# Performance work log

Measured on AMD Instinct MI355X. Metric: run time of the kernel, lower is better.

## Reference

```python
import jax, jax.numpy as jnp
import numpy as np

BATCH = 16384
IN = 1024
OUT = 1024
SIGMA_MIN = 0.1
SIGMA_MAX = 1.0


def setup_inputs() -> dict:
    key = jax.random.key(0)
    k0, k1, k2, k3 = jax.random.split(key, 4)
    x = jax.random.normal(k0, (BATCH, IN), dtype=jnp.float32)
    # torch init: triu(randn) -> upper-triangular reflector banks
    U = jnp.triu(jax.random.normal(k1, (IN, IN), dtype=jnp.float32))
    V = jnp.triu(jax.random.normal(k2, (OUT, OUT), dtype=jnp.float32))
    p = 0.001 * jax.random.normal(k3, (min(IN, OUT),), dtype=jnp.float32)
    bias = jnp.zeros((OUT,), dtype=jnp.float32)
    return {"x": x, "U": U, "V": V, "p": p, "bias": bias}


def _hprod_step(x, u):
    # u has zeros in its first i entries (triu row i), so the full-vector
    # form equals torch's sliced Hprod on the last k = n - i columns.
    alpha = 2.0 * (x @ u) / jnp.dot(u, u)          # [bs]
    return x - alpha[:, None] * u[None, :], None   # rank-1 update


def reference(x, U, V, p, bias):
    r = (SIGMA_MAX - SIGMA_MIN) / 2.0
    sigma_mean = SIGMA_MIN + r
    # mask enforces torch slice semantics (entries below diag never used)
    Um = U * jnp.triu(jnp.ones_like(U))
    Vm = V * jnp.triu(jnp.ones_like(V))
    # Umultiply: reflectors i = 0 .. n_U-1 in order (sequential recurrence)
    x, _ = jax.lax.scan(_hprod_step, x, Um)
    # Sigma: diagonal scaling (square case IN == OUT)
    sigmas = 2.0 * r * (jax.nn.sigmoid(p) - 0.5) + sigma_mean
    x = x * sigmas[None, :]
    # Vmultiply: reflectors i = n_V-1 .. 0 (reverse order)
    x, _ = jax.lax.scan(_hprod_step, x, Vm[::-1])
    return x + bias
```

## Files before the change

### kernel.cpp

```cpp
#include <hip/hip_runtime.h>
#include <stdint.h>

typedef __attribute__((ext_vector_type(8))) short short8;
typedef __attribute__((ext_vector_type(4))) float f32x4;

#define NN 1024
#define NBATCH 16384
#define ME ((size_t)NN * NN)
#define AS1 (const __attribute__((address_space(1))) void*)
#define AS3 (__attribute__((address_space(3))) void*)

__device__ __forceinline__ unsigned short f32_to_bf16_rne(float f) {
  unsigned int u = __float_as_uint(f);
  unsigned int r = (u + 0x7fffu + ((u >> 16) & 1u)) >> 16;
  return (unsigned short)r;
}

__device__ __forceinline__ unsigned int pack2bf(float lo, float hi) {
  return (unsigned int)f32_to_bf16_rne(lo) | ((unsigned int)f32_to_bf16_rne(hi) << 16);
}

__device__ __forceinline__ void split_bf16(float x, unsigned short& h, unsigned short& l) {
  h = f32_to_bf16_rne(x);
  float hf = __uint_as_float((unsigned int)h << 16);
  l = f32_to_bf16_rne(x - hf);
}

__device__ __forceinline__ float allsum64(float x) {
  x += __int_as_float(__builtin_amdgcn_update_dpp(0, __float_as_int(x), 0xB1, 0xF, 0xF, true));
  x += __int_as_float(__builtin_amdgcn_update_dpp(0, __float_as_int(x), 0x4E, 0xF, 0xF, true));
  x += __int_as_float(__builtin_amdgcn_update_dpp(0, __float_as_int(x), 0x141, 0xF, 0xF, true));
  x += __int_as_float(__builtin_amdgcn_update_dpp(0, __float_as_int(x), 0x140, 0xF, 0xF, true));
#if __has_builtin(__builtin_amdgcn_permlane16_swap) && __has_builtin(__builtin_amdgcn_permlane32_swap)
  {
    auto r16 = __builtin_amdgcn_permlane16_swap(__float_as_uint(x), __float_as_uint(x), false, false);
    x = __uint_as_float(r16[0]) + __uint_as_float(r16[1]);
    auto r32 = __builtin_amdgcn_permlane32_swap(__float_as_uint(x), __float_as_uint(x), false, false);
    x = __uint_as_float(r32[0]) + __uint_as_float(r32[1]);
  }
#else
  x += __int_as_float(__builtin_amdgcn_ds_swizzle(__float_as_int(x), 0x401F));
  x += __shfl_xor(x, 32);
#endif
  return x;
}

__global__ __launch_bounds__(256) void prep_kernel(
    const float* __restrict__ U, const float* __restrict__ V,
    const float* __restrict__ p, float* __restrict__ tau_u,
    float* __restrict__ tau_v, float* __restrict__ sigmas) {
  int wave = threadIdx.x >> 6, lane = threadIdx.x & 63;
  int row = blockIdx.x * 4 + wave;
  if (row < 2048) {
    const float* u = (row < NN) ? (U + (size_t)row * NN) : (V + (size_t)(row - NN) * NN);
    float s = 0.f;
#pragma unroll
    for (int t = 0; t < 16; ++t) { float a = u[lane + (t << 6)]; s += a * a; }
    s = allsum64(s);
    if (lane == 0) {
      float tau = 2.0f / s;
      if (row < NN) tau_u[row] = tau;
      else tau_v[row - NN] = tau;
    }
  } else if (row < 2064) {
    int j = ((row - 2048) << 6) + lane;
    float pj = p[j];
    float sg = 1.0f / (1.0f + expf(-pj));
    sigmas[j] = 0.9f * (sg - 0.5f) + 0.55f;
  }
}

__global__ __launch_bounds__(256) void castx_kernel(
    const float* __restrict__ X, unsigned short* __restrict__ Xb) {
  const size_t n4 = (size_t)NBATCH * NN / 4;
  for (size_t i = (size_t)blockIdx.x * 256 + threadIdx.x; i < n4; i += (size_t)gridDim.x * 256) {
    float4 v = reinterpret_cast<const float4*>(X)[i];
    uint2 o;
    o.x = pack2bf(v.x, v.y);
    o.y = pack2bf(v.z, v.w);
    reinterpret_cast<uint2*>(Xb)[i] = o;
  }
}

__global__ __launch_bounds__(64) void gram_t8_kernel(
    const float* __restrict__ U, const float* __restrict__ V,
    const float* __restrict__ tau_u, const float* __restrict__ tau_v,
    float* __restrict__ T8all) {
  __shared__ float G[64];
  const int blk = blockIdx.x;
  const int lane = threadIdx.x;
  const float* bank;
  int rbase, rsign, st;
  if (blk < 128) { bank = U; rbase = 8 * blk; rsign = 1; st = 8 * blk; }
  else { int s = blk - 128; bank = V; rbase = 1023 - 8 * s; rsign = -1; st = 1016 - 8 * s; }

  if (lane < 28) {
    int j = 1, k = 0, t = lane;
    for (int jj = 1; jj < 8; ++jj) {
      int lo = jj * (jj - 1) / 2, hi = jj * (jj + 1) / 2;
      if (t >= lo && t < hi) { j = jj; k = t - lo; }
    }
    const float* rk = bank + (size_t)(rbase + rsign * k) * NN;
    const float* rj = bank + (size_t)(rbase + rsign * j) * NN;
    float acc = 0.f;
    for (int i = st >> 2; i < 256; ++i) {
      float4 a = *reinterpret_cast<const float4*>(rk + 4 * i);
      float4 b = *reinterpret_cast<const float4*>(rj + 4 * i);
      acc += a.x * b.x + a.y * b.y + a.z * b.z + a.w * b.w;
    }
    G[k * 8 + j] = acc;
  }
  __syncthreads();

  if (lane < 8) {
    float Tr[8];
#pragma unroll
    for (int j = 0; j < 8; ++j) Tr[j] = 0.f;
#pragma unroll
    for (int j = 0; j < 8; ++j) {
      int grow = rbase + rsign * j;
      float tj = (blk < 128) ? tau_u[grow] : tau_v[grow];
      float a = 0.f;
#pragma unroll
      for (int k = 0; k < 8; ++k) {
        if (k < j) a += Tr[k] * G[k * 8 + j];
      }
      Tr[j] = (lane == j) ? tj : (-tj * a);
    }
#pragma unroll
    for (int j = 0; j < 8; ++j) T8all[(size_t)blk * 64 + lane * 8 + j] = Tr[j];
  }
}

__global__ __launch_bounds__(256) void splity_kernel(
    const float* __restrict__ U, const float* __restrict__ V,
    unsigned short* __restrict__ Yhi, unsigned short* __restrict__ Ylo,
    unsigned short* __restrict__ YThi, unsigned short* __restrict__ YTlo) {
  __shared__ float ys[128][129];
  const int tid = threadIdx.x;
  const int c = blockIdx.x >> 3, et = blockIdx.x & 7;
  const int half = tid & 1;
  const int slot = tid >> 1;
  const int e0 = et << 7;
  const int grow = (c < 8) ? ((c << 7) + slot) : (1023 - ((c - 8) << 7) - slot);
  const float* src = ((c < 8) ? U : V) + (size_t)grow * NN + e0 + (half << 6);
#pragma unroll
  for (int i = 0; i < 16; ++i) {
    float4 v4 = *reinterpret_cast<const float4*>(src + (i << 2));
    const int kk = (half << 6) + (i << 2);
    ys[slot][kk + 0] = v4.x; ys[slot][kk + 1] = v4.y;
    ys[slot][kk + 2] = v4.z; ys[slot][kk + 3] = v4.w;
  }
  __syncthreads();
  {
    const size_t rbase = ((size_t)(c * 128 + slot)) * NN + e0 + (half << 6);
#pragma unroll
    for (int i = 0; i < 16; ++i) {
      const int kk = (half << 6) + (i << 2);
      ushort4 h4, l4;
      split_bf16(ys[slot][kk + 0], h4.x, l4.x);
      split_bf16(ys[slot][kk + 1], h4.y, l4.y);
      split_bf16(ys[slot][kk + 2], h4.z, l4.z);
      split_bf16(ys[slot][kk + 3], h4.w, l4.w);
      *reinterpret_cast<ushort4*>(&Yhi[rbase + (i << 2)]) = h4;
      *reinterpret_cast<ushort4*>(&Ylo[rbase + (i << 2)]) = l4;
    }
  }
  {
    const int e = slot;
    const size_t tbase = ((size_t)c * 1024 + e0 + e) * 128 + (half << 6);
#pragma unroll
    for (int i = 0; i < 16; ++i) {
      const int k0 = (half << 6) + (i << 2);
      ushort4 h4, l4;
      split_bf16(ys[k0 + 0][e], h4.x, l4.x);
      split_bf16(ys[k0 + 1][e], h4.y, l4.y);
      split_bf16(ys[k0 + 2][e], h4.z, l4.z);
      split_bf16(ys[k0 + 3][e], h4.w, l4.w);
      *reinterpret_cast<ushort4*>(&YThi[tbase + (i << 2)]) = h4;
      *reinterpret_cast<ushort4*>(&YTlo[tbase + (i << 2)]) = l4;
    }
  }
}

#define LDK 40
#define BM 128
#define BN 128
#define BK 32

__global__ __launch_bounds__(256) void gramt_kernel(
    const unsigned short* __restrict__ Yhi, const unsigned short* __restrict__ Ylo,
    float* __restrict__ Gp) {
  const int tid = threadIdx.x;
  const int c = blockIdx.x >> 3, ks = blockIdx.x & 7;
  const bool productive = (c < 8) ? (ks >= c) : (ks >= 7 - (c - 8));
  if (!productive) {
    float4 z = {0.f, 0.f, 0.f, 0.f};
    float4* dst = reinterpret_cast<float4*>(Gp + (((size_t)c * 8 + ks) << 14));
    for (int i = tid; i < 4096; i += 256) dst[i] = z;
    return;
  }
  __shared__ unsigned short Hs[128 * LDK];
  __shared__ unsigned short Ls[128 * LDK];
  const int lane = tid & 63, wave = tid >> 6;
  const int wm = wave & 1, wn = wave >> 1;
  const int srow = tid >> 1, scol = (tid & 1) << 4;
  const unsigned short* ph = Yhi + ((size_t)(c * 128 + srow)) * NN + ks * 128 + scol;
  const unsigned short* pl = Ylo + ((size_t)(c * 128 + srow)) * NN + ks * 128 + scol;

  f32x4 acc[4][4];
#pragma unroll
  for (int a = 0; a < 4; ++a)
#pragma unroll
    for (int b = 0; b < 4; ++b) acc[a][b] = 0.f;

  const int arow0 = wm * 64, brow0 = wn * 64;
  const int fr = lane & 15, kb = (lane >> 4) << 3;

#pragma unroll 1
  for (int kt = 0; kt < 4; ++kt) {
    __syncthreads();
    *reinterpret_cast<uint4*>(&Hs[srow * LDK + scol]) = *reinterpret_cast<const uint4*>(ph + kt * 32);
    *reinterpret_cast<uint4*>(&Hs[srow * LDK + scol + 8]) = *reinterpret_cast<const uint4*>(ph + kt * 32 + 8);
    *reinterpret_cast<uint4*>(&Ls[srow * LDK + scol]) = *reinterpret_cast<const uint4*>(pl + kt * 32);
    *reinterpret_cast<uint4*>(&Ls[srow * LDK + scol + 8]) = *reinterpret_cast<const uint4*>(pl + kt * 32 + 8);
    __syncthreads();
    short8 ah[4], al[4], bh[4], bl[4];
#pragma unroll
    for (int tr = 0; tr < 4; ++tr) {
      ah[tr] = *reinterpret_cast<const short8*>(&Hs[(arow0 + tr * 16 + fr) * LDK + kb]);
      al[tr] = *reinterpret_cast<const short8*>(&Ls[(arow0 + tr * 16 + fr) * LDK + kb]);
    }
#pragma unroll
    for (int tc = 0; tc < 4; ++tc) {
      bh[tc] = *reinterpret_cast<const short8*>(&Hs[(brow0 + tc * 16 + fr) * LDK + kb]);
      bl[tc] = *reinterpret_cast<const short8*>(&Ls[(brow0 + tc * 16 + fr) * LDK + kb]);
    }
#pragma unroll
    for (int tr = 0; tr < 4; ++tr)
#pragma unroll
      for (int tc = 0; tc < 4; ++tc) {
        acc[tr][tc] = __builtin_amdgcn_mfma_f32_16x16x32_bf16(ah[tr], bh[tc], acc[tr][tc], 0, 0, 0);
        acc[tr][tc] = __builtin_amdgcn_mfma_f32_16x16x32_bf16(ah[tr], bl[tc], acc[tr][tc], 0, 0, 0);
        acc[tr][tc] = __builtin_amdgcn_mfma_f32_16x16x32_bf16(al[tr], bh[tc], acc[tr][tc], 0, 0, 0);
      }
  }
  const int rq = (lane >> 4) << 2;
#pragma unroll
  for (int tc = 0; tc < 4; ++tc) {
    const int gc = brow0 + tc * 16 + fr;
#pragma unroll
    for (int tr = 0; tr < 4; ++tr) {
      const int gr = arow0 + tr * 16 + rq;
#pragma unroll
      for (int q = 0; q < 4; ++q)
        Gp[(((size_t)c * 8 + ks) * 128 + gr + q) * 128 + gc] = acc[tr][tc][q];
    }
  }
}

__global__ __launch_bounds__(256) void gsum_tinit_kernel(
    const float* __restrict__ Gp, const float* __restrict__ T8all,
    float* __restrict__ G, float* __restrict__ Tg) {
  const int bid = blockIdx.x;
  if (bid < 1024) {
    const size_t i = (size_t)bid * 256 + threadIdx.x;
    const size_t c = i >> 14, rc = i & 16383;
    float s = 0.f;
#pragma unroll
    for (int sl = 0; sl < 8; ++sl)
      s += Gp[(c * 8 + sl) * 16384 + rc];
    G[i] = s;
  } else {
    const size_t base = ((size_t)(bid - 1024) * 256 + threadIdx.x) * 16;
#pragma unroll 1
    for (int e = 0; e < 16; ++e) {
      const size_t i = base + e;
      const int c = (int)(i >> 14), rc = (int)(i & 16383);
      const int r = rc >> 7, cl = rc & 127;
      float v = 0.f;
      if ((r >> 3) == (cl >> 3)) {
        const int sb = r >> 3;
        const int t8i = (c < 8) ? (16 * c + sb) : (128 + 16 * (c - 8) + sb);
        v = T8all[(size_t)t8i * 64 + (r & 7) * 8 + (cl & 7)];
      }
      Tg[i] = v;
    }
  }
}

template <int B>
__global__ __launch_bounds__(256) void tmerge_kernel(
    const float* __restrict__ G, float* __restrict__ Tg) {
  __shared__ float T1s[B * B], T2s[B * B], Gs[B * B], Xs[B * B];
  const int nm = 128 / (2 * B);
  const int c = blockIdx.x / nm, m = blockIdx.x % nm;
  const int a0 = 2 * B * m;
  const int tid = threadIdx.x;
  float* Tc = Tg + (size_t)c * 16384;
  for (int i = tid; i < B * B; i += 256) {
    const int r = i / B, cl = i % B;
    T1s[i] = Tc[(a0 + r) * 128 + a0 + cl];
    T2s[i] = Tc[(a0 + B + r) * 128 + a0 + B + cl];
    Gs[i] = G[((size_t)c * 128 + a0 + r) * 128 + a0 + B + cl];
  }
  __syncthreads();
  for (int i = tid; i < B * B; i += 256) {
    const int r = i / B, cl = i % B;
    float s = 0.f;
    for (int k = 0; k <= cl; ++k) s += Gs[r * B + k] * T2s[k * B + cl];
    Xs[i] = s;
  }
  __syncthreads();
  for (int i = tid; i < B * B; i += 256) {
    const int r = i / B, cl = i % B;
    float s = 0.f;
    for (int k = r; k < B; ++k) s -= T1s[r * B + k] * Xs[k * B + cl];
    Tc[(a0 + r) * 128 + a0 + B + cl] = s;
  }
}

__global__ __launch_bounds__(256) void tsplit_kernel(
    const float* __restrict__ Tg, unsigned short* __restrict__ Thi,
    unsigned short* __restrict__ Tlo) {
  const size_t i0 = ((size_t)blockIdx.x * 256 + threadIdx.x) * 16;
#pragma unroll
  for (int v = 0; v < 4; ++v) {
    float4 t = *reinterpret_cast<const float4*>(Tg + i0 + 4 * v);
    ushort4 h4, l4;
    split_bf16(t.x, h4.x, l4.x);
    split_bf16(t.y, h4.y, l4.y);
    split_bf16(t.z, h4.z, l4.z);
    split_bf16(t.w, h4.w, l4.w);
    *reinterpret_cast<ushort4*>(&Thi[i0 + 4 * v]) = h4;
    *reinterpret_cast<ushort4*>(&Tlo[i0 + 4 * v]) = l4;
  }
}

__global__ __launch_bounds__(256) void zw_kernel(
    const unsigned short* __restrict__ Thi, const unsigned short* __restrict__ Tlo,
    const unsigned short* __restrict__ YThi, const unsigned short* __restrict__ YTlo,
    unsigned short* __restrict__ WThi, unsigned short* __restrict__ WTlo) {
  __shared__ unsigned short Xh[128 * LDK], Xl[128 * LDK];
  __shared__ unsigned short Wh[128 * LDK], Wl[128 * LDK];
  const int tid = threadIdx.x;
  const int lane = tid & 63, wave = tid >> 6;
  const int c = blockIdx.x >> 3, bn = blockIdx.x & 7;
  const int n0 = bn * 128;
  const int wm = wave & 1, wn = wave >> 1;
  const int srow = tid >> 1, scol = (tid & 1) << 4;
  const unsigned short* pxh = Thi + ((size_t)c * 128 + srow) * 128 + scol;
  const unsigned short* pxl = Tlo + ((size_t)c * 128 + srow) * 128 + scol;
  const unsigned short* pwh = YThi + ((size_t)c * 1024 + n0 + srow) * 128 + scol;
  const unsigned short* pwl = YTlo + ((size_t)c * 1024 + n0 + srow) * 128 + scol;

  f32x4 acc[4][4];
#pragma unroll
  for (int a = 0; a < 4; ++a)
#pragma unroll
    for (int b = 0; b < 4; ++b) acc[a][b] = 0.f;

  const int arow0 = wm * 64, brow0 = wn * 64;
  const int fr = lane & 15, kb = (lane >> 4) << 3;

#pragma unroll 1
  for (int kt = 0; kt < 4; ++kt) {
    __syncthreads();
    *reinterpret_cast<uint4*>(&Xh[srow * LDK + scol]) = *reinterpret_cast<const uint4*>(pxh + kt * 32);
    *reinterpret_cast<uint4*>(&Xh[srow * LDK + scol + 8]) = *reinterpret_cast<const uint4*>(pxh + kt * 32 + 8);
    *reinterpret_cast<uint4*>(&Xl[srow * LDK + scol]) = *reinterpret_cast<const uint4*>(pxl + kt * 32);
    *reinterpret_cast<uint4*>(&Xl[srow * LDK + scol + 8]) = *reinterpret_cast<const uint4*>(pxl + kt * 32 + 8);
    *reinterpret_cast<uint4*>(&Wh[srow * LDK + scol]) = *reinterpret_cast<const uint4*>(pwh + kt * 32);
    *reinterpret_cast<uint4*>(&Wh[srow * LDK + scol + 8]) = *reinterpret_cast<const uint4*>(pwh + kt * 32 + 8);
    *reinterpret_cast<uint4*>(&Wl[srow * LDK + scol]) = *reinterpret_cast<const uint4*>(pwl + kt * 32);
    *reinterpret_cast<uint4*>(&Wl[srow * LDK + scol + 8]) = *reinterpret_cast<const uint4*>(pwl + kt * 32 + 8);
    __syncthreads();
    short8 ah[4], al[4], bh[4], bl[4];
#pragma unroll
    for (int tr = 0; tr < 4; ++tr) {
      ah[tr] = *reinterpret_cast<const short8*>(&Xh[(arow0 + tr * 16 + fr) * LDK + kb]);
      al[tr] = *reinterpret_cast<const short8*>(&Xl[(arow0 + tr * 16 + fr) * LDK + kb]);
    }
#pragma unroll
    for (int tc = 0; tc < 4; ++tc) {
      bh[tc] = *reinterpret_cast<const short8*>(&Wh[(brow0 + tc * 16 + fr) * LDK + kb]);
      bl[tc] = *reinterpret_cast<const short8*>(&Wl[(brow0 + tc * 16 + fr) * LDK + kb]);
    }
#pragma unroll
    for (int tr = 0; tr < 4; ++tr)
#pragma unroll
      for (int tc = 0; tc < 4; ++tc) {
        acc[tr][tc] = __builtin_amdgcn_mfma_f32_16x16x32_bf16(ah[tr], bh[tc], acc[tr][tc], 0, 0, 0);
        acc[tr][tc] = __builtin_amdgcn_mfma_f32_16x16x32_bf16(ah[tr], bl[tc], acc[tr][tc], 0, 0, 0);
        acc[tr][tc] = __builtin_amdgcn_mfma_f32_16x16x32_bf16(al[tr], bh[tc], acc[tr][tc], 0, 0, 0);
      }
  }
  const int rq = (lane >> 4) << 2;
#pragma unroll
  for (int tc = 0; tc < 4; ++tc) {
    const int gc = brow0 + tc * 16 + fr;
#pragma unroll
    for (int tr = 0; tr < 4; ++tr) {
      const int gr = arow0 + tr * 16 + rq;
      ushort4 h4, l4;
      split_bf16(acc[tr][tc][0], h4.x, l4.x);
      split_bf16(acc[tr][tc][1], h4.y, l4.y);
      split_bf16(acc[tr][tc][2], h4.z, l4.z);
      split_bf16(acc[tr][tc][3], h4.w, l4.w);
      const size_t off = ((size_t)c * 1024 + n0 + gc) * 128 + gr;
      *reinterpret_cast<ushort4*>(&WThi[off]) = h4;
      *reinterpret_cast<ushort4*>(&WTlo[off]) = l4;
    }
  }
}

__global__ __launch_bounds__(256) void chainc_kernel(
    const unsigned short* __restrict__ YThi, const unsigned short* __restrict__ YTlo,
    const unsigned short* __restrict__ WThi, const unsigned short* __restrict__ WTlo,
    unsigned short* __restrict__ chains) {
  const int tid = threadIdx.x;
  const int lane = tid & 63, wave = tid >> 6;
  const int c = blockIdx.x >> 6, b6 = blockIdx.x & 63;
  const int bm = b6 & 7, bn = b6 >> 3;
  const int m0 = bm * 128, n0 = bn * 128;
  const int wm = wave & 1, wn = wave >> 1;
  const int arow0 = wm * 64, brow0 = wn * 64;
  const int fr = lane & 15, kb = (lane >> 4) << 3;
  const int rq = (lane >> 4) << 2;
  unsigned short* dst = chains + (size_t)c * ME;

  const int z0 = (c < 8) ? (128 * c) : (896 - 128 * (c - 8));
  if (m0 < z0 || n0 < z0) {
    if ((c & 1) == 0) {
#pragma unroll
      for (int tc = 0; tc < 4; ++tc) {
        const int gcg = n0 + brow0 + tc * 16 + fr;
#pragma unroll
        for (int tr = 0; tr < 4; ++tr) {
          const int grg = m0 + arow0 + tr * 16 + rq;
#pragma unroll
          for (int q = 0; q < 4; ++q)
            dst[(size_t)(grg + q) * NN + gcg] = f32_to_bf16_rne((grg + q) == gcg ? 1.0f : 0.0f);
        }
      }
    } else {
#pragma unroll
      for (int tc = 0; tc < 4; ++tc) {
        const int gcg = n0 + brow0 + tc * 16 + fr;
#pragma unroll
        for (int tr = 0; tr < 4; ++tr) {
          const int grg = m0 + arow0 + tr * 16 + rq;
          ushort4 pk;
          pk.x = f32_to_bf16_rne((grg + 0) == gcg ? 1.0f : 0.0f);
          pk.y = f32_to_bf16_rne((grg + 1) == gcg ? 1.0f : 0.0f);
          pk.z = f32_to_bf16_rne((grg + 2) == gcg ? 1.0f : 0.0f);
          pk.w = f32_to_bf16_rne((grg + 3) == gcg ? 1.0f : 0.0f);
          *reinterpret_cast<ushort4*>(&dst[(size_t)gcg * NN + grg]) = pk;
        }
      }
    }
    return;
  }

  __shared__ unsigned short Xh[128 * LDK], Xl[128 * LDK];
  __shared__ unsigned short Wh[128 * LDK], Wl[128 * LDK];
  const int srow = tid >> 1, scol = (tid & 1) << 4;
  const unsigned short* pxh = YThi + ((size_t)c * 1024 + m0 + srow) * 128 + scol;
  const unsigned short* pxl = YTlo + ((size_t)c * 1024 + m0 + srow) * 128 + scol;
  const unsigned short* pwh = WThi + ((size_t)c * 1024 + n0 + srow) * 128 + scol;
  const unsigned short* pwl = WTlo + ((size_t)c * 1024 + n0 + srow) * 128 + scol;

  f32x4 acc[4][4];
#pragma unroll
  for (int a = 0; a < 4; ++a)
#pragma unroll
    for (int b = 0; b < 4; ++b) acc[a][b] = 0.f;

#pragma unroll 1
  for (int kt = 0; kt < 4; ++kt) {
    __syncthreads();
    *reinterpret_cast<uint4*>(&Xh[srow * LDK + scol]) = *reinterpret_cast<const uint4*>(pxh + kt * 32);
    *reinterpret_cast<uint4*>(&Xh[srow * LDK + scol + 8]) = *reinterpret_cast<const uint4*>(pxh + kt * 32 + 8);
    *reinterpret_cast<uint4*>(&Xl[srow * LDK + scol]) = *reinterpret_cast<const uint4*>(pxl + kt * 32);
    *reinterpret_cast<uint4*>(&Xl[srow * LDK + scol + 8]) = *reinterpret_cast<const uint4*>(pxl + kt * 32 + 8);
    *reinterpret_cast<uint4*>(&Wh[srow * LDK + scol]) = *reinterpret_cast<const uint4*>(pwh + kt * 32);
    *reinterpret_cast<uint4*>(&Wh[srow * LDK + scol + 8]) = *reinterpret_cast<const uint4*>(pwh + kt * 32 + 8);
    *reinterpret_cast<uint4*>(&Wl[srow * LDK + scol]) = *reinterpret_cast<const uint4*>(pwl + kt * 32);
    *reinterpret_cast<uint4*>(&Wl[srow * LDK + scol + 8]) = *reinterpret_cast<const uint4*>(pwl + kt * 32 + 8);
    __syncthreads();
    short8 ah[4], al[4], bh[4], bl[4];
#pragma unroll
    for (int tr = 0; tr < 4; ++tr) {
      ah[tr] = *reinterpret_cast<const short8*>(&Xh[(arow0 + tr * 16 + fr) * LDK + kb]);
      al[tr] = *reinterpret_cast<const short8*>(&Xl[(arow0 + tr * 16 + fr) * LDK + kb]);
    }
#pragma unroll
    for (int tc = 0; tc < 4; ++tc) {
      bh[tc] = *reinterpret_cast<const short8*>(&Wh[(brow0 + tc * 16 + fr) * LDK + kb]);
      bl[tc] = *reinterpret_cast<const short8*>(&Wl[(brow0 + tc * 16 + fr) * LDK + kb]);
    }
#pragma unroll
    for (int tr = 0; tr < 4; ++tr)
#pragma unroll
      for (int tc = 0; tc < 4; ++tc) {
        acc[tr][tc] = __builtin_amdgcn_mfma_f32_16x16x32_bf16(ah[tr], bh[tc], acc[tr][tc], 0, 0, 0);
        acc[tr][tc] = __builtin_amdgcn_mfma_f32_16x16x32_bf16(ah[tr], bl[tc], acc[tr][tc], 0, 0, 0);
        acc[tr][tc] = __builtin_amdgcn_mfma_f32_16x16x32_bf16(al[tr], bh[tc], acc[tr][tc], 0, 0, 0);
      }
  }
  if ((c & 1) == 0) {
#pragma unroll
    for (int tc = 0; tc < 4; ++tc) {
      const int gcg = n0 + brow0 + tc * 16 + fr;
#pragma unroll
      for (int tr = 0; tr < 4; ++tr) {
        const int grg = m0 + arow0 + tr * 16 + rq;
#pragma unroll
        for (int q = 0; q < 4; ++q) {
          const float val = ((grg + q) == gcg ? 1.0f : 0.0f) - acc[tr][tc][q];
          dst[(size_t)(grg + q) * NN + gcg] = f32_to_bf16_rne(val);
        }
      }
    }
  } else {
#pragma unroll
    for (int tc = 0; tc < 4; ++tc) {
      const int gcg = n0 + brow0 + tc * 16 + fr;
#pragma unroll
      for (int tr = 0; tr < 4; ++tr) {
        const int grg = m0 + arow0 + tr * 16 + rq;
        ushort4 pk;
        pk.x = f32_to_bf16_rne(((grg + 0) == gcg ? 1.0f : 0.0f) - acc[tr][tc][0]);
        pk.y = f32_to_bf16_rne(((grg + 1) == gcg ? 1.0f : 0.0f) - acc[tr][tc][1]);
        pk.z = f32_to_bf16_rne(((grg + 2) == gcg ? 1.0f : 0.0f) - acc[tr][tc][2]);
        pk.w = f32_to_bf16_rne(((grg + 3) == gcg ? 1.0f : 0.0f) - acc[tr][tc][3]);
        *reinterpret_cast<ushort4*>(&dst[(size_t)gcg * NN + grg]) = pk;
      }
    }
  }
}

__device__ __forceinline__ void cb_stage(
    const unsigned short* __restrict__ agbase, const unsigned short* __restrict__ bgbase,
    unsigned short* __restrict__ la, unsigned short* __restrict__ lb, int tid, int kt) {
#pragma unroll
  for (int i = 0; i < 2; ++i) {
    const int slot = tid + 256 * i;
    const int row = slot >> 2, s = slot & 3;
    const int cs = s ^ ((row >> 1) & 3);
    __builtin_amdgcn_global_load_lds(
        AS1(agbase + (size_t)row * NN + kt * 32 + cs * 8), AS3(la + row * 32 + s * 8), 16, 0, 0);
  }
#pragma unroll
  for (int i = 0; i < 2; ++i) {
    const int slot = tid + 256 * i;
    const int row = slot >> 2, s = slot & 3;
    const int cs = s ^ ((row >> 1) & 3);
    __builtin_amdgcn_global_load_lds(
        AS1(bgbase + (size_t)row * NN + kt * 32 + cs * 8), AS3(lb + row * 32 + s * 8), 16, 0, 0);
  }
}

__device__ __forceinline__ void cb_compute(
    const unsigned short* __restrict__ As, const unsigned short* __restrict__ Bs,
    f32x4 acc[4][4], int arow0, int brow0, int fr, int kb) {
  short8 af[4], bf[4];
  const int ck = kb >> 3;
#pragma unroll
  for (int tr = 0; tr < 4; ++tr) {
    const int row = arow0 + tr * 16 + fr;
    const int sl = ck ^ ((row >> 1) & 3);
    af[tr] = *reinterpret_cast<const short8*>(&As[row * 32 + sl * 8]);
  }
#pragma unroll
  for (int tc = 0; tc < 4; ++tc) {
    const int row = brow0 + tc * 16 + fr;
    const int sl = ck ^ ((row >> 1) & 3);
    bf[tc] = *reinterpret_cast<const short8*>(&Bs[row * 32 + sl * 8]);
  }
#pragma unroll
  for (int tr = 0; tr < 4; ++tr)
#pragma unroll
    for (int tc = 0; tc < 4; ++tc)
      acc[tr][tc] = __builtin_amdgcn_mfma_f32_16x16x32_bf16(af[tr], bf[tc], acc[tr][tc], 0, 0, 0);
}

__device__ __forceinline__ void compose_body(
    const unsigned short* __restrict__ Xb, const unsigned short* __restrict__ Wb,
    unsigned short* __restrict__ Op, const float* __restrict__ sig, int b, bool tstore,
    int z0) {
  const int tid = threadIdx.x;
  const int lane = tid & 63, wave = tid >> 6;
  const int bm = b & 7, bn = b >> 3;
  const int m0 = bm * BM, n0 = bn * BN;
  const int wm = wave & 1, wn = wave >> 1;
  const int arow0 = wm * 64, brow0 = wn * 64;
  const int fr = lane & 15, kb = (lane >> 4) << 3;
  const int rq = (lane >> 4) << 2;

  if (m0 < z0 || n0 < z0) {
    if (!tstore) {
#pragma unroll
      for (int tc = 0; tc < 4; ++tc) {
        const int gc = n0 + brow0 + tc * 16 + fr;
        const float s = sig ? sig[gc] : 1.0f;
#pragma unroll
        for (int tr = 0; tr < 4; ++tr) {
          const int gr = m0 + arow0 + tr * 16 + rq;
#pragma unroll
          for (int q = 0; q < 4; ++q)
            Op[(size_t)(gr + q) * NN + gc] = f32_to_bf16_rne((gr + q == gc) ? s : 0.0f);
        }
      }
    } else {
#pragma unroll
      for (int tc = 0; tc < 4; ++tc) {
        const int gc = n0 + brow0 + tc * 16 + fr;
#pragma unroll
        for (int tr = 0; tr < 4; ++tr) {
          const int gr = m0 + arow0 + tr * 16 + rq;
          ushort4 pk;
          pk.x = f32_to_bf16_rne((gr + 0 == gc) ? 1.0f : 0.0f);
          pk.y = f32_to_bf16_rne((gr + 1 == gc) ? 1.0f : 0.0f);
          pk.z = f32_to_bf16_rne((gr + 2 == gc) ? 1.0f : 0.0f);
          pk.w = f32_to_bf16_rne((gr + 3 == gc) ? 1.0f : 0.0f);
          *reinterpret_cast<ushort4*>(&Op[(size_t)gc * NN + gr]) = pk;
        }
      }
    }
    return;
  }

  __shared__ unsigned short As[3][BM * 32];
  __shared__ unsigned short Bs[3][BN * 32];
  f32x4 acc[4][4];
#pragma unroll
  for (int a = 0; a < 4; ++a)
#pragma unroll
    for (int bb = 0; bb < 4; ++bb) acc[a][bb] = 0.f;

  const unsigned short* agbase = Xb + (size_t)m0 * NN;
  const unsigned short* bgbase = Wb + (size_t)n0 * NN;

  cb_stage(agbase, bgbase, &As[0][0], &Bs[0][0], tid, 0);
  cb_stage(agbase, bgbase, &As[1][0], &Bs[1][0], tid, 1);
#pragma unroll 1
  for (int kt = 0; kt < 31; ++kt) {
    asm volatile("s_waitcnt vmcnt(4)" ::: "memory");
    __builtin_amdgcn_s_barrier();
    __builtin_amdgcn_sched_barrier(0);
    if (kt + 2 < 32) {
      const int nb = (kt + 2) % 3;
      cb_stage(agbase, bgbase, &As[nb][0], &Bs[nb][0], tid, kt + 2);
    }
    cb_compute(&As[kt % 3][0], &Bs[kt % 3][0], acc, arow0, brow0, fr, kb);
  }
  asm volatile("s_waitcnt vmcnt(0)" ::: "memory");
  __builtin_amdgcn_s_barrier();
  __builtin_amdgcn_sched_barrier(0);
  cb_compute(&As[1][0], &Bs[1][0], acc, arow0, brow0, fr, kb);

  if (!tstore) {
#pragma unroll
    for (int tc = 0; tc < 4; ++tc) {
      const int gc = n0 + brow0 + tc * 16 + fr;
      const float s = sig ? sig[gc] : 1.0f;
#pragma unroll
      for (int tr = 0; tr < 4; ++tr) {
        const int gr = m0 + arow0 + tr * 16 + rq;
#pragma unroll
        for (int q = 0; q < 4; ++q) {
          Op[(size_t)(gr + q) * NN + gc] = f32_to_bf16_rne(acc[tr][tc][q] * s);
        }
      }
    }
  } else {
#pragma unroll
    for (int tc = 0; tc < 4; ++tc) {
      const int gc = n0 + brow0 + tc * 16 + fr;
#pragma unroll
      for (int tr = 0; tr < 4; ++tr) {
        const int gr = m0 + arow0 + tr * 16 + rq;
        ushort4 pk;
        pk.x = f32_to_bf16_rne(acc[tr][tc][0]);
        pk.y = f32_to_bf16_rne(acc[tr][tc][1]);
        pk.z = f32_to_bf16_rne(acc[tr][tc][2]);
        pk.w = f32_to_bf16_rne(acc[tr][tc][3]);
        *reinterpret_cast<ushort4*>(&Op[(size_t)gc * NN + gr]) = pk;
      }
    }
  }
}

__global__ __launch_bounds__(256) void composeL1_kernel(
    const unsigned short* __restrict__ ch, unsigned short* __restrict__ P) {
  const int sub = blockIdx.x >> 6, b = blockIdx.x & 63;
  const int i = sub & 3;
  const unsigned short* x = ch + (size_t)((sub < 4 ? 0 : 8) + 2 * i) * ME;
  const int z0 = (sub < 4) ? (256 * i) : (768 - 256 * i);
  compose_body(x, x + ME, P + (size_t)sub * ME, nullptr, b, (i & 1) != 0, z0);
}

__global__ __launch_bounds__(256) void composeL2_kernel(
    const unsigned short* __restrict__ P, unsigned short* __restrict__ Q) {
  const int sub = blockIdx.x >> 6, b = blockIdx.x & 63;
  const int z0 = (sub == 1 || sub == 2) ? 512 : 0;
  compose_body(P + (size_t)(2 * sub) * ME, P + (size_t)(2 * sub + 1) * ME,
               Q + (size_t)sub * ME, nullptr, b, (sub & 1) != 0, z0);
}

__global__ __launch_bounds__(256) void composeL3_kernel(
    const unsigned short* __restrict__ Q, const float* __restrict__ sigmas,
    unsigned short* __restrict__ F) {
  const int sub = blockIdx.x >> 6, b = blockIdx.x & 63;
  if (sub == 0) compose_body(Q, Q + ME, F, sigmas, b, false, 0);
  else compose_body(Q + 2 * ME, Q + 3 * ME, F + ME, nullptr, b, true, 0);
}

__global__ __launch_bounds__(256) void composeL4_kernel(
    const unsigned short* __restrict__ F, unsigned short* __restrict__ Mt) {
  compose_body(F + ME, F, Mt, nullptr, blockIdx.x, false, 0);
}

__global__ __launch_bounds__(512) void gemm256_kernel(
    const unsigned short* __restrict__ Xb, const unsigned short* __restrict__ Mt,
    const float* __restrict__ bias, float* __restrict__ Out) {
  __shared__ unsigned short As[3][256 * 32];
  __shared__ unsigned short Bs[3][128 * 32];
  const int tid = threadIdx.x;
  const int lane = tid & 63, wave = tid >> 6;
  const int bm = blockIdx.x & 63, bn = blockIdx.x >> 6;
  const int m0 = bm * 256, n0 = bn * 128;
  const int wm = wave & 3, wn = wave >> 2;
  const int arow0 = wm * 64, brow0 = wn * 64;
  const int fr = lane & 15, kb = (lane >> 4) << 3;

  f32x4 acc[4][4];
#pragma unroll
  for (int a = 0; a < 4; ++a)
#pragma unroll
    for (int b = 0; b < 4; ++b) acc[a][b] = 0.f;

  const unsigned short* agbase = Xb + (size_t)m0 * NN;
  const unsigned short* bgbase = Mt + (size_t)n0 * NN;

#define G256_STAGE(B, KT)                                                        \
  {                                                                              \
    _Pragma("unroll")                                                            \
    for (int i = 0; i < 2; ++i) {                                                \
      const int slot = tid + 512 * i;                                            \
      const int row = slot >> 2, s = slot & 3;                                   \
      const int cs = s ^ ((row >> 1) & 3);                                       \
      __builtin_amdgcn_global_load_lds(                                          \
          AS1(agbase + (size_t)row * NN + (KT) * 32 + cs * 8),                   \
          AS3(&As[B][row * 32 + s * 8]), 16, 0, 0);                              \
    }                                                                            \
    {                                                                            \
      const int row = tid >> 2, s = tid & 3;                                     \
      const int cs = s ^ ((row >> 1) & 3);                                       \
      __builtin_amdgcn_global_load_lds(                                          \
          AS1(bgbase + (size_t)row * NN + (KT) * 32 + cs * 8),                   \
          AS3(&Bs[B][row * 32 + s * 8]), 16, 0, 0);                              \
    }                                                                            \
  }

#define G256_CMP(B)                                                              \
  {                                                                              \
    short8 af[4], bf4[4];                                                        \
    const int ck = kb >> 3;                                                      \
    _Pragma("unroll")                                                            \
    for (int tr = 0; tr < 4; ++tr) {                                             \
      const int row = arow0 + tr * 16 + fr;                                      \
      const int sl = ck ^ ((row >> 1) & 3);                                      \
      af[tr] = *reinterpret_cast<const short8*>(&As[B][row * 32 + sl * 8]);      \
    }                                                                            \
    _Pragma("unroll")                                                            \
    for (int tc = 0; tc < 4; ++tc) {                                             \
      const int row = brow0 + tc * 16 + fr;                                      \
      const int sl = ck ^ ((row >> 1) & 3);                                      \
      bf4[tc] = *reinterpret_cast<const short8*>(&Bs[B][row * 32 + sl * 8]);     \
    }                                                                            \
    _Pragma("unroll")                                                            \
    for (int tr = 0; tr < 4; ++tr)                                               \
      _Pragma("unroll")                                                          \
      for (int tc = 0; tc < 4; ++tc)                                             \
        acc[tr][tc] = __builtin_amdgcn_mfma_f32_16x16x32_bf16(af[tr], bf4[tc], acc[tr][tc], 0, 0, 0); \
  }

  G256_STAGE(0, 0)
  G256_STAGE(1, 1)
#pragma unroll 1
  for (int kt = 0; kt < 31; ++kt) {
    asm volatile("s_waitcnt vmcnt(3)" ::: "memory");
    __builtin_amdgcn_s_barrier();
    __builtin_amdgcn_sched_barrier(0);
    if (kt + 2 < 32) {
      const int nb = (kt + 2) % 3;
      G256_STAGE(nb, kt + 2)
    }
    G256_CMP(kt % 3)
  }
  asm volatile("s_waitcnt vmcnt(0)" ::: "memory");
  __builtin_amdgcn_s_barrier();
  __builtin_amdgcn_sched_barrier(0);
  G256_CMP(1)
#undef G256_STAGE
#undef G256_CMP

  const int rq = (lane >> 4) << 2;
#pragma unroll
  for (int tc = 0; tc < 4; ++tc) {
    const int gc = n0 + brow0 + tc * 16 + fr;
    const float bv = bias[gc];
#pragma unroll
    for (int tr = 0; tr < 4; ++tr) {
      const int gr = m0 + arow0 + tr * 16 + rq;
#pragma unroll
      for (int q = 0; q < 4; ++q) {
        Out[(size_t)(gr + q) * NN + gc] = acc[tr][tc][q] + bv;
      }
    }
  }
}

__global__ __launch_bounds__(256) void gemm_fb_kernel(
    const float* __restrict__ X, const unsigned short* __restrict__ Mt,
    const float* __restrict__ bias, float* __restrict__ Out) {
  __shared__ float Af[2][BM * 32];
  __shared__ unsigned short Bsl[2][BN * 32];
  const int tid = threadIdx.x;
  const int lane = tid & 63, wave = tid >> 6;
  const int bm = blockIdx.x & 127;
  const int bn = blockIdx.x >> 7;
  const int m0 = bm * BM, n0 = bn * BN;
  const int wm = wave & 1, wn = wave >> 1;
  const int arow0 = wm * 64, brow0 = wn * 64;
  const int fr = lane & 15, kb = (lane >> 4) << 3;

  f32x4 acc[4][4];
#pragma unroll
  for (int a = 0; a < 4; ++a)
#pragma unroll
    for (int b = 0; b < 4; ++b) acc[a][b] = 0.f;

  const float* agbase = X + (size_t)m0 * NN;
  const unsigned short* bgbase = Mt + (size_t)n0 * NN;

#define FB_STAGE(PB, KT)                                                        \
  {                                                                             \
    _Pragma("unroll")                                                           \
    for (int i = 0; i < 4; ++i) {                                               \
      const int slot = tid + 256 * i;                                           \
      const int row = slot >> 3, s = slot & 7;                                  \
      __builtin_amdgcn_global_load_lds(                                         \
          AS1(agbase + (size_t)row * NN + (KT) * 32 + s * 4),                   \
          AS3(&Af[PB][row * 32 + s * 4]), 16, 0, 0);                            \
    }                                                                           \
    _Pragma("unroll")                                                           \
    for (int i = 0; i < 2; ++i) {                                               \
      const int slot = tid + 256 * i;                                           \
      const int row = slot >> 2, s = slot & 3;                                  \
      __builtin_amdgcn_global_load_lds(                                         \
          AS1(bgbase + (size_t)row * NN + (KT) * 32 + s * 8),                   \
          AS3(&Bsl[PB][row * 32 + s * 8]), 16, 0, 0);                           \
    }                                                                           \
  }

  FB_STAGE(0, 0)
  int pb = 0;
#pragma unroll 1
  for (int kt = 0; kt < 32; ++kt) {
    __syncthreads();
    if (kt + 1 < 32) FB_STAGE(pb ^ 1, kt + 1)
    {
      short8 af[4], bf[4];
      const int c0 = kb >> 2;
#pragma unroll
      for (int tr = 0; tr < 4; ++tr) {
        const int row = arow0 + tr * 16 + fr;
        const f32x4 a0 = *reinterpret_cast<const f32x4*>(&Af[pb][row * 32 + c0 * 4]);
        const f32x4 a1 = *reinterpret_cast<const f32x4*>(&Af[pb][row * 32 + (c0 + 1) * 4]);
        uint4 w;
        w.x = pack2bf(a0[0], a0[1]); w.y = pack2bf(a0[2], a0[3]);
        w.z = pack2bf(a1[0], a1[1]); w.w = pack2bf(a1[2], a1[3]);
        af[tr] = *reinterpret_cast<const short8*>(&w);
      }
#pragma unroll
      for (int tc = 0; tc < 4; ++tc) {
        const int row = brow0 + tc * 16 + fr;
        bf[tc] = *reinterpret_cast<const short8*>(&Bsl[pb][row * 32 + kb]);
      }
#pragma unroll
      for (int tr = 0; tr < 4; ++tr)
#pragma unroll
        for (int tc = 0; tc < 4; ++tc)
          acc[tr][tc] = __builtin_amdgcn_mfma_f32_16x16x32_bf16(af[tr], bf[tc], acc[tr][tc], 0, 0, 0);
    }
    pb ^= 1;
  }
#undef FB_STAGE

  const int rq = (lane >> 4) << 2;
#pragma unroll
  for (int tc = 0; tc < 4; ++tc) {
    const int gc = n0 + brow0 + tc * 16 + fr;
    const float bv = bias[gc];
#pragma unroll
    for (int tr = 0; tr < 4; ++tr) {
      const int gr = m0 + arow0 + tr * 16 + rq;
#pragma unroll
      for (int q = 0; q < 4; ++q) {
        Out[(size_t)(gr + q) * NN + gc] = acc[tr][tc][q] + bv;
      }
    }
  }
}

extern "C" void kernel_launch(void* const* d_in, const int* in_sizes, int n_in,
                              void* d_out, int out_size, void* d_ws, size_t ws_size,
                              hipStream_t stream) {
  const float* x = (const float*)d_in[0];
  const float* U = (const float*)d_in[1];
  const float* V = (const float*)d_in[2];
  const float* p = (const float*)d_in[3];
  const float* bias = (const float*)d_in[4];
  float* out = (float*)d_out;

  char* ws = (char*)d_ws;
  float* tau_u = (float*)(ws);
  float* tau_v = (float*)(ws + 4096);
  float* sigmas = (float*)(ws + 8192);
  float* T8all = (float*)(ws + 16384);
  unsigned short* Mt = (unsigned short*)(ws + 81920);

  const size_t XB_OFF = 4u * 1024 * 1024;
  const size_t XB_BYTES = (size_t)NBATCH * NN * 2;
  const bool fast = ws_size >= XB_OFF + XB_BYTES;
  unsigned short* Xb = (unsigned short*)(ws + XB_OFF);

  unsigned short* sc = (unsigned short*)d_out;
  unsigned short* chains = sc;
  unsigned short* P = sc + 16 * ME;
  unsigned short* Q = sc + 24 * ME;
  unsigned short* F = sc + 28 * ME;
  unsigned short* YThi = sc + 16 * ME;
  unsigned short* YTlo = sc + 18 * ME;
  unsigned short* WThi = sc + 20 * ME;
  unsigned short* WTlo = sc + 22 * ME;
  unsigned short* Yhi = sc + 24 * ME;
  unsigned short* Ylo = sc + 26 * ME;
  float* Gp = (float*)(sc + 28 * ME);
  float* G = (float*)sc;
  float* Tg = (float*)(sc + ME);
  unsigned short* Thi = sc + 24 * ME;
  unsigned short* Tlo = Thi + 262144;

  prep_kernel<<<516, 256, 0, stream>>>(U, V, p, tau_u, tau_v, sigmas);
  if (fast) castx_kernel<<<2048, 256, 0, stream>>>(x, Xb);
  gram_t8_kernel<<<256, 64, 0, stream>>>(U, V, tau_u, tau_v, T8all);
  splity_kernel<<<128, 256, 0, stream>>>(U, V, Yhi, Ylo, YThi, YTlo);
  gramt_kernel<<<128, 256, 0, stream>>>(Yhi, Ylo, Gp);
  gsum_tinit_kernel<<<1088, 256, 0, stream>>>(Gp, T8all, G, Tg);
  tmerge_kernel<8><<<128, 256, 0, stream>>>(G, Tg);
  tmerge_kernel<16><<<64, 256, 0, stream>>>(G, Tg);
  tmerge_kernel<32><<<32, 256, 0, stream>>>(G, Tg);
  tmerge_kernel<64><<<16, 256, 0, stream>>>(G, Tg);
  tsplit_kernel<<<64, 256, 0, stream>>>(Tg, Thi, Tlo);
  zw_kernel<<<128, 256, 0, stream>>>(Thi, Tlo, YThi, YTlo, WThi, WTlo);
  chainc_kernel<<<1024, 256, 0, stream>>>(YThi, YTlo, WThi, WTlo, chains);
  composeL1_kernel<<<512, 256, 0, stream>>>(chains, P);
  composeL2_kernel<<<256, 256, 0, stream>>>(P, Q);
  composeL3_kernel<<<128, 256, 0, stream>>>(Q, sigmas, F);
  composeL4_kernel<<<64, 256, 0, stream>>>(F, Mt);
  if (fast) gemm256_kernel<<<512, 512, 0, stream>>>(Xb, Mt, bias, out);
  else gemm_fb_kernel<<<1024, 256, 0, stream>>>(x, Mt, bias, out);
}
```

Measured before the change: 318.1 us.

## Split-K the late compose GEMMs and skip zero leading K-tiles

```diff
diff --git a/kernel.cpp b/kernel.cpp
--- a/kernel.cpp
+++ b/kernel.cpp
@@ -585,6 +585,29 @@
       acc[tr][tc] = __builtin_amdgcn_mfma_f32_16x16x32_bf16(af[tr], bf[tc], acc[tr][tc], 0, 0, 0);
 }
 
+__device__ __forceinline__ void compose_core(
+    const unsigned short* __restrict__ agbase, const unsigned short* __restrict__ bgbase,
+    unsigned short (*As)[BM * 32], unsigned short (*Bs)[BN * 32],
+    f32x4 acc[4][4], int tid, int arow0, int brow0, int fr, int kb, int kt0, int nk) {
+  cb_stage(agbase, bgbase, &As[0][0], &Bs[0][0], tid, kt0);
+  if (nk >= 2) cb_stage(agbase, bgbase, &As[1][0], &Bs[1][0], tid, kt0 + 1);
+#pragma unroll 1
+  for (int i = 0; i < nk - 1; ++i) {
+    asm volatile("s_waitcnt vmcnt(4)" ::: "memory");
+    __builtin_amdgcn_s_barrier();
+    __builtin_amdgcn_sched_barrier(0);
+    if (i + 2 < nk) {
+      const int nb = (i + 2) % 3;
+      cb_stage(agbase, bgbase, &As[nb][0], &Bs[nb][0], tid, kt0 + i + 2);
+    }
+    cb_compute(&As[i % 3][0], &Bs[i % 3][0], acc, arow0, brow0, fr, kb);
+  }
+  asm volatile("s_waitcnt vmcnt(0)" ::: "memory");
+  __builtin_amdgcn_s_barrier();
+  __builtin_amdgcn_sched_barrier(0);
+  cb_compute(&As[(nk - 1) % 3][0], &Bs[(nk - 1) % 3][0], acc, arow0, brow0, fr, kb);
+}
+
 __device__ __forceinline__ void compose_body(
     const unsigned short* __restrict__ Xb, const unsigned short* __restrict__ Wb,
     unsigned short* __restrict__ Op, const float* __restrict__ sig, int b, bool tstore,
@@ -639,26 +662,10 @@
 #pragma unroll
     for (int bb = 0; bb < 4; ++bb) acc[a][bb] = 0.f;
 
-  const unsigned short* agbase = Xb + (size_t)m0 * NN;
-  const unsigned short* bgbase = Wb + (size_t)n0 * NN;
-
-  cb_stage(agbase, bgbase, &As[0][0], &Bs[0][0], tid, 0);
-  cb_stage(agbase, bgbase, &As[1][0], &Bs[1][0], tid, 1);
-#pragma unroll 1
-  for (int kt = 0; kt < 31; ++kt) {
-    asm volatile("s_waitcnt vmcnt(4)" ::: "memory");
-    __builtin_amdgcn_s_barrier();
-    __builtin_amdgcn_sched_barrier(0);
-    if (kt + 2 < 32) {
-      const int nb = (kt + 2) % 3;
-      cb_stage(agbase, bgbase, &As[nb][0], &Bs[nb][0], tid, kt + 2);
-    }
-    cb_compute(&As[kt % 3][0], &Bs[kt % 3][0], acc, arow0, brow0, fr, kb);
-  }
-  asm volatile("s_waitcnt vmcnt(0)" ::: "memory");
-  __builtin_amdgcn_s_barrier();
-  __builtin_amdgcn_sched_barrier(0);
-  cb_compute(&As[1][0], &Bs[1][0], acc, arow0, brow0, fr, kb);
+  const int kt0 = z0 >> 5;
+  const int nk = 32 - kt0;
+  compose_core(Xb + (size_t)m0 * NN, Wb + (size_t)n0 * NN, As, Bs, acc,
+               tid, arow0, brow0, fr, kb, kt0, nk);
 
   if (!tstore) {
 #pragma unroll
@@ -692,6 +699,55 @@
   }
 }
 
+__device__ __forceinline__ void compose_ks_body(
+    const unsigned short* __restrict__ Xb, const unsigned short* __restrict__ Wb,
+    float* __restrict__ Pp, int b, bool tstore, int slice) {
+  const int tid = threadIdx.x;
+  const int lane = tid & 63, wave = tid >> 6;
+  const int bm = b & 7, bn = b >> 3;
+  const int m0 = bm * BM, n0 = bn * BN;
+  const int wm = wave & 1, wn = wave >> 1;
+  const int arow0 = wm * 64, brow0 = wn * 64;
+  const int fr = lane & 15, kb = (lane >> 4) << 3;
+  const int rq = (lane >> 4) << 2;
+
+  __shared__ unsigned short As[3][BM * 32];
+  __shared__ unsigned short Bs[3][BN * 32];
+  f32x4 acc[4][4];
+#pragma unroll
+  for (int a = 0; a < 4; ++a)
+#pragma unroll
+    for (int bb = 0; bb < 4; ++bb) acc[a][bb] = 0.f;
+
+  compose_core(Xb + (size_t)m0 * NN, Wb + (size_t)n0 * NN, As, Bs, acc,
+               tid, arow0, brow0, fr, kb, slice * 16, 16);
+
+  if (!tstore) {
+#pragma unroll
+    for (int tc = 0; tc < 4; ++tc) {
+      const int gc = n0 + brow0 + tc * 16 + fr;
+#pragma unroll
+      for (int tr = 0; tr < 4; ++tr) {
+        const int gr = m0 + arow0 + tr * 16 + rq;
+#pragma unroll
+        for (int q = 0; q < 4; ++q)
+          Pp[(size_t)(gr + q) * NN + gc] = acc[tr][tc][q];
+      }
+    }
+  } else {
+#pragma unroll
+    for (int tc = 0; tc < 4; ++tc) {
+      const int gc = n0 + brow0 + tc * 16 + fr;
+#pragma unroll
+      for (int tr = 0; tr < 4; ++tr) {
+        const int gr = m0 + arow0 + tr * 16 + rq;
+        float4 v = {acc[tr][tc][0], acc[tr][tc][1], acc[tr][tc][2], acc[tr][tc][3]};
+        *reinterpret_cast<float4*>(&Pp[(size_t)gc * NN + gr]) = v;
+      }
+    }
+  }
+}
+
 __global__ __launch_bounds__(256) void composeL1_kernel(
     const unsigned short* __restrict__ ch, unsigned short* __restrict__ P) {
   const int sub = blockIdx.x >> 6, b = blockIdx.x & 63;
@@ -709,17 +765,34 @@
                Q + (size_t)sub * ME, nullptr, b, (sub & 1) != 0, z0);
 }
 
-__global__ __launch_bounds__(256) void composeL3_kernel(
-    const unsigned short* __restrict__ Q, const float* __restrict__ sigmas,
-    unsigned short* __restrict__ F) {
-  const int sub = blockIdx.x >> 6, b = blockIdx.x & 63;
-  if (sub == 0) compose_body(Q, Q + ME, F, sigmas, b, false, 0);
-  else compose_body(Q + 2 * ME, Q + 3 * ME, F + ME, nullptr, b, true, 0);
-}
-
-__global__ __launch_bounds__(256) void composeL4_kernel(
-    const unsigned short* __restrict__ F, unsigned short* __restrict__ Mt) {
-  compose_body(F + ME, F, Mt, nullptr, blockIdx.x, false, 0);
+__global__ __launch_bounds__(256) void composeL3ks_kernel(
+    const unsigned short* __restrict__ Q, float* __restrict__ P32) {
+  const int sub = blockIdx.x >> 7, slice = (blockIdx.x >> 6) & 1, b = blockIdx.x & 63;
+  const unsigned short* X = Q + (size_t)(2 * sub) * ME;
+  const unsigned short* W = Q + (size_t)(2 * sub + 1) * ME;
+  compose_ks_body(X, W, P32 + (size_t)(sub * 2 + slice) * ME, b, sub == 1, slice);
+}
+
+__global__ __launch_bounds__(256) void composeL4ks_kernel(
+    const unsigned short* __restrict__ F, float* __restrict__ P32) {
+  const int slice = blockIdx.x >> 6, b = blockIdx.x & 63;
+  compose_ks_body(F + ME, F, P32 + (size_t)slice * ME, b, false, slice);
+}
+
+__global__ __launch_bounds__(256) void reduce2_kernel(
+    const float* __restrict__ p0, const float* __restrict__ p1,
+    const float* __restrict__ sig, unsigned short* __restrict__ out) {
+  const size_t i4 = (size_t)blockIdx.x * 256 + threadIdx.x;
+  float4 a = reinterpret_cast<const float4*>(p0)[i4];
+  float4 b = reinterpret_cast<const float4*>(p1)[i4];
+  float4 s = {1.f, 1.f, 1.f, 1.f};
+  if (sig) s = *reinterpret_cast<const float4*>(&sig[(i4 * 4) & 1023]);
+  ushort4 o;
+  o.x = f32_to_bf16_rne((a.x + b.x) * s.x);
+  o.y = f32_to_bf16_rne((a.y + b.y) * s.y);
+  o.z = f32_to_bf16_rne((a.z + b.z) * s.z);
+  o.w = f32_to_bf16_rne((a.w + b.w) * s.w);
+  reinterpret_cast<ushort4*>(out)[i4] = o;
 }
 
 __global__ __launch_bounds__(512) void gemm256_kernel(
@@ -954,6 +1027,8 @@
   float* Tg = (float*)(sc + ME);
   unsigned short* Thi = sc + 24 * ME;
   unsigned short* Tlo = Thi + 262144;
+  float* P32L3 = (float*)sc;
+  float* P32L4 = (float*)(sc + 8 * ME);
 
   prep_kernel<<<516, 256, 0, stream>>>(U, V, p, tau_u, tau_v, sigmas);
   if (fast) castx_kernel<<<2048, 256, 0, stream>>>(x, Xb);
@@ -970,8 +1045,11 @@
   chainc_kernel<<<1024, 256, 0, stream>>>(YThi, YTlo, WThi, WTlo, chains);
   composeL1_kernel<<<512, 256, 0, stream>>>(chains, P);
   composeL2_kernel<<<256, 256, 0, stream>>>(P, Q);
-  composeL3_kernel<<<128, 256, 0, stream>>>(Q, sigmas, F);
-  composeL4_kernel<<<64, 256, 0, stream>>>(F, Mt);
+  composeL3ks_kernel<<<256, 256, 0, stream>>>(Q, P32L3);
+  reduce2_kernel<<<1024, 256, 0, stream>>>(P32L3, P32L3 + ME, sigmas, F);
+  reduce2_kernel<<<1024, 256, 0, stream>>>(P32L3 + 2 * ME, P32L3 + 3 * ME, nullptr, F + ME);
+  composeL4ks_kernel<<<128, 256, 0, stream>>>(F, P32L4);
+  reduce2_kernel<<<1024, 256, 0, stream>>>(P32L4, P32L4 + ME, nullptr, Mt);
   if (fast) gemm256_kernel<<<512, 512, 0, stream>>>(Xb, Mt, bias, out);
   else gemm_fb_kernel<<<1024, 256, 0, stream>>>(x, Mt, bias, out);
 }
```

Measured after the change: 302.6 us. 1.05x faster.
